# Kernel tuning notes

Measured on AMD Instinct MI355X. Metric: run time of the kernel, lower is better.

The kernel has to match this reference:

```python
import jax, jax.numpy as jnp
import numpy as np

B, S, D = 8, 4096, 256
N_INTENT, N_SLOT = 512, 1024


def setup_inputs() -> dict:
    key = jax.random.key(0)
    k1, k2, k3, k4 = jax.random.split(key, 4)
    return {
        "input_intent": jax.random.normal(k1, (B, S, D), dtype=jnp.float32),
        "input_slot": jax.random.normal(k2, (B, S, D), dtype=jnp.float32),
        "mask": jnp.ones((B, S), dtype=jnp.int32),  # unused, kept for API fidelity
        "W_intent_emb": jax.random.normal(k3, (N_INTENT, D), dtype=jnp.float32) * 0.02,
        "W_slot_emb": jax.random.normal(k4, (N_SLOT, D), dtype=jnp.float32) * 0.02,
    }


def reference(input_intent, input_slot, mask, W_intent_emb, W_slot_emb):
    # scores: [B, S, N] = hidden @ label_table^T
    intent_probs = jax.nn.softmax(jnp.einsum("bsd,nd->bsn", input_intent, W_intent_emb), axis=-1)
    slot_probs = jax.nn.softmax(jnp.einsum("bsd,nd->bsn", input_slot, W_slot_emb), axis=-1)
    # weighted sum over label embeddings: [B, S, D]
    intent_res = jnp.einsum("bsn,nd->bsd", intent_probs, W_intent_emb)
    slot_res = jnp.einsum("bsn,nd->bsd", slot_probs, W_slot_emb)
    return (intent_res, slot_res)
```

## Files before the change

### kernel.cpp

```cpp
#include <hip/hip_runtime.h>


#define TM 128
#define DD 256
#define THREADS 512
#define TOK 32768

typedef __bf16 bf16t;
typedef bf16t v8bf __attribute__((ext_vector_type(8)));
typedef float v16f __attribute__((ext_vector_type(16)));

#define WT0   0
#define WT1   32768
#define W20   65536
#define W21   98304
#define P_OFF 131072
#define L_OFF 147456
#define LDS_BYTES 147968

#define IWT 0
#define SWT 262144
#define IW2 786432
#define SW2 1048576

__device__ __forceinline__ unsigned short f2bf(float x) {
    unsigned u = __builtin_bit_cast(unsigned, x);
    unsigned r = u + 0x7fffu + ((u >> 16) & 1u);
    return (unsigned short)(r >> 16);
}

__global__ __launch_bounds__(256) void prep_w_kernel(
    const float* __restrict__ w_int, const float* __restrict__ w_slot,
    char* __restrict__ wsb)
{
    int t = blockIdx.x * 256 + threadIdx.x;
    int w = t >> 6, lane = t & 63;
    int hi = lane >> 5, l5 = lane & 31;
    union { unsigned short u[8]; uint4 q; } pk;

    if (w < 768) {
        int st   = (w >= 256);
        int widx = w - (st ? 256 : 0);
        int it = widx >> 5, fid = widx & 31;
        int wc = fid >> 4, kk = fid & 15;
        const float* W = st ? w_slot : w_int;
        int n  = it * 64 + wc * 32 + l5;
        int k0 = kk * 16 + hi * 8;
        #pragma unroll
        for (int j = 0; j < 8; ++j) pk.u[j] = f2bf(W[(size_t)n * DD + k0 + j]);
        char* dst = wsb + (st ? SWT : IWT) + (size_t)it * 32768 + fid * 1024 + lane * 16;
        *(uint4*)dst = pk.q;
    } else {
        int w2 = w - 768;
        int st   = (w2 >= 256);
        int widx = w2 - (st ? 256 : 0);
        int it = widx >> 5, fid = widx & 31;
        int kb = fid >> 3, db = fid & 7;
        const float* W = st ? w_slot : w_int;
        int n0 = it * 64 + kb * 16 + hi * 8;
        int d  = db * 32 + l5;
        #pragma unroll
        for (int j = 0; j < 8; ++j) pk.u[j] = f2bf(W[(size_t)(n0 + j) * DD + d]);
        char* dst = wsb + (st ? SW2 : IW2) + (size_t)it * 32768 + fid * 1024 + lane * 16;
        *(uint4*)dst = pk.q;
    }
}

__global__ __launch_bounds__(THREADS)
__attribute__((amdgpu_waves_per_eu(2, 2)))
void label_attn_kernel(
    const float* __restrict__ in_intent,
    const float* __restrict__ in_slot,
    const char* __restrict__ wsb,
    float* __restrict__ out)
{
    extern __shared__ char lds[];

    const int tid  = threadIdx.x;
    const int lane = tid & 63;
    const int wid  = tid >> 6;
    const int wr   = wid >> 1;
    const int wc   = wid & 1;
    const int hi   = lane >> 5;
    const int l5   = lane & 31;
    const int t0   = blockIdx.x * TM;

    float* lsf = (float*)(lds + L_OFF);

    const int kbl_w = (l5 >> 4) & 1;
    const int hb_w  = (l5 >> 3) & 1;
    const int pw_base = P_OFF + wr * 4096 + (wc * 2 + kbl_w) * 1024 + (l5 & 7) * 2;
    const int pw_sxor = (kbl_w << 2) ^ (hb_w << 1);

    for (int st = 0; st < 2; ++st) {
        __builtin_amdgcn_s_barrier();
        if (tid < TM) lsf[tid] = 0.0f;

        const float* __restrict__ inp = st ? in_slot : in_intent;
        const char*  __restrict__ wtg = wsb + (st ? SWT : IWT);
        const char*  __restrict__ w2g = wsb + (st ? SW2 : IW2);
        const int niter = st ? 16 : 8;
        float* __restrict__ outp = out + (size_t)st * TOK * DD;

        v8bf h[16];
        {
            const float* hp = inp + (size_t)(t0 + wr * 32 + l5) * DD + hi * 8;
            #pragma unroll
            for (int kk = 0; kk < 16; ++kk) {
                float4 a = *(const float4*)(hp + kk * 16);
                float4 b = *(const float4*)(hp + kk * 16 + 4);
                union { unsigned short u[8]; v8bf v; } pk;
                pk.u[0] = f2bf(a.x); pk.u[1] = f2bf(a.y);
                pk.u[2] = f2bf(a.z); pk.u[3] = f2bf(a.w);
                pk.u[4] = f2bf(b.x); pk.u[5] = f2bf(b.y);
                pk.u[6] = f2bf(b.z); pk.u[7] = f2bf(b.w);
                h[kk] = pk.v;
            }
        }

        #pragma unroll
        for (int c = 0; c < 4; ++c) {
            int chunk = wid * 4 + c;
            __builtin_amdgcn_global_load_lds(
                (const __attribute__((address_space(1))) unsigned*)(wtg + chunk * 1024 + lane * 16),
                (__attribute__((address_space(3))) unsigned*)(lds + WT0 + chunk * 1024),
                16, 0, 0);
        }
        __builtin_amdgcn_sched_barrier(0);
        #pragma unroll
        for (int c = 0; c < 4; ++c) {
            int chunk = wid * 4 + c;
            __builtin_amdgcn_global_load_lds(
                (const __attribute__((address_space(1))) unsigned*)(w2g + chunk * 1024 + lane * 16),
                (__attribute__((address_space(3))) unsigned*)(lds + W20 + chunk * 1024),
                16, 0, 0);
        }
        __builtin_amdgcn_sched_barrier(0);
        asm volatile("s_waitcnt vmcnt(0)" ::: "memory");
        __builtin_amdgcn_sched_barrier(0);
        __builtin_amdgcn_s_barrier();

        v16f  o[4] = {};
        float ls[16] = {};

        for (int it = 0; it < niter; ++it) {
            const int cur = it & 1;
            char* wt_buf = lds + (cur ? WT1 : WT0);
            char* w2_buf = lds + (cur ? W21 : W20);

            if (it + 1 < niter) {
                const char* s1 = wtg + (size_t)(it + 1) * 32768;
                const char* s2 = w2g + (size_t)(it + 1) * 32768;
                char* d1 = lds + (cur ? WT0 : WT1);
                char* d2 = lds + (cur ? W20 : W21);
                #pragma unroll
                for (int c = 0; c < 4; ++c) {
                    int chunk = wid * 4 + c;
                    __builtin_amdgcn_global_load_lds(
                        (const __attribute__((address_space(1))) unsigned*)(s1 + chunk * 1024 + lane * 16),
                        (__attribute__((address_space(3))) unsigned*)(d1 + chunk * 1024),
                        16, 0, 0);
                }
                __builtin_amdgcn_sched_barrier(0);
                #pragma unroll
                for (int c = 0; c < 4; ++c) {
                    int chunk = wid * 4 + c;
                    __builtin_amdgcn_global_load_lds(
                        (const __attribute__((address_space(1))) unsigned*)(s2 + chunk * 1024 + lane * 16),
                        (__attribute__((address_space(3))) unsigned*)(d2 + chunk * 1024),
                        16, 0, 0);
                }
                __builtin_amdgcn_sched_barrier(0);
            }

            v16f c0 = {}, c1 = {};
            #pragma unroll
            for (int kk = 0; kk < 16; kk += 2) {
                v8bf b0 = *(const v8bf*)(wt_buf + (wc * 16 + kk) * 1024 + lane * 16);
                v8bf b1 = *(const v8bf*)(wt_buf + (wc * 16 + kk + 1) * 1024 + lane * 16);
                c0 = __builtin_amdgcn_mfma_f32_32x32x16_bf16(h[kk],     b0, c0, 0, 0, 0);
                c1 = __builtin_amdgcn_mfma_f32_32x32x16_bf16(h[kk + 1], b1, c1, 0, 0, 0);
            }
            v16f cacc = c0 + c1;

            #pragma unroll
            for (int r = 0; r < 16; ++r) {
                int tl = (r & 3) + 8 * (r >> 2) + 4 * hi;
                float e = __expf(cacc[r]);
                unsigned short ub = f2bf(e);
                ls[r] += __builtin_bit_cast(float, ((unsigned)ub) << 16);
                int slot = (tl + 32 * hb_w) ^ pw_sxor;
                *(unsigned short*)(lds + pw_base + slot * 16) = ub;
            }

            if (it + 1 < niter) {
                asm volatile("s_waitcnt vmcnt(8)" ::: "memory");
            } else {
                asm volatile("s_waitcnt vmcnt(0)" ::: "memory");
            }
            asm volatile("s_waitcnt lgkmcnt(0)" ::: "memory");
            __builtin_amdgcn_sched_barrier(0);
            __builtin_amdgcn_s_barrier();

            #pragma unroll
            for (int kb = 0; kb < 4; ++kb) {
                int sl = lane ^ ((kb & 1) << 2) ^ (hi << 1);
                v8bf pa = *(const v8bf*)(lds + P_OFF + wr * 4096 + kb * 1024 + sl * 16);
                #pragma unroll
                for (int db = 0; db < 4; ++db) {
                    v8bf wb = *(const v8bf*)(w2_buf + (kb * 8 + wc * 4 + db) * 1024 + lane * 16);
                    o[db] = __builtin_amdgcn_mfma_f32_32x32x16_bf16(pa, wb, o[db], 0, 0, 0);
                }
            }

            if (it + 1 < niter) {
                asm volatile("s_waitcnt vmcnt(4)" ::: "memory");
            }
            __builtin_amdgcn_sched_barrier(0);
            __builtin_amdgcn_s_barrier();
        }

        #pragma unroll
        for (int r = 0; r < 16; ++r) {
            float s = ls[r];
            s += __shfl_xor(s, 1);
            s += __shfl_xor(s, 2);
            s += __shfl_xor(s, 4);
            s += __shfl_xor(s, 8);
            s += __shfl_xor(s, 16);
            ls[r] = s;
        }
        if (l5 == 0) {
            #pragma unroll
            for (int r = 0; r < 16; ++r) {
                int tl = (r & 3) + 8 * (r >> 2) + 4 * hi;
                atomicAdd(&lsf[wr * 32 + tl], ls[r]);
            }
        }
        __syncthreads();

        #pragma unroll
        for (int r = 0; r < 16; ++r) {
            int tl = (r & 3) + 8 * (r >> 2) + 4 * hi;
            float inv = 1.0f / lsf[wr * 32 + tl];
            size_t row = (size_t)(t0 + wr * 32 + tl);
            #pragma unroll
            for (int db = 0; db < 4; ++db)
                outp[row * DD + wc * 128 + db * 32 + l5] = o[db][r] * inv;
        }
    }
}

extern "C" void kernel_launch(void* const* d_in, const int* in_sizes, int n_in,
                              void* d_out, int out_size, void* d_ws, size_t ws_size,
                              hipStream_t stream) {
    const float* in_intent = (const float*)d_in[0];
    const float* in_slot   = (const float*)d_in[1];
    const float* w_intent  = (const float*)d_in[3];
    const float* w_slot    = (const float*)d_in[4];
    float* out = (float*)d_out;
    char* wsb = (char*)d_ws;

    (void)hipFuncSetAttribute((const void*)label_attn_kernel,
                              hipFuncAttributeMaxDynamicSharedMemorySize, LDS_BYTES);

    prep_w_kernel<<<384, 256, 0, stream>>>(w_intent, w_slot, wsb);

    label_attn_kernel<<<dim3(TOK / TM, 1, 1), dim3(THREADS, 1, 1), LDS_BYTES, stream>>>(
        in_intent, in_slot, wsb, out);
}
```

Baseline: 179.3 us.

## Keep softmax probabilities in registers via lane shuffles, split N across wave pairs

Computes the score tile transposed (weights as A operand) so each lane's exp'd probabilities can be packed and exchanged with a cross-half shuffle to form the second MFMA's A operand directly. This removes the P round trip through LDS and one barrier per iteration. Each wave pair now splits the label dimension rather than the output D dimension, so each wave accumulates all 256 output columns (twice the accumulator registers) and the halves are reduced through LDS at the end. The weight prefetch is issued before the input conversion, and the per-iteration wait becomes a full vmcnt(0), which may expose prefetch latency and raise register pressure.

```diff
diff --git a/kernel.cpp b/kernel.cpp
--- a/kernel.cpp
+++ b/kernel.cpp
@@ -14,9 +14,8 @@
 #define WT1   32768
 #define W20   65536
 #define W21   98304
-#define P_OFF 131072
-#define L_OFF 147456
-#define LDS_BYTES 147968
+#define L_OFF 131072
+#define LDS_BYTES 131584
 
 #define IWT 0
 #define SWT 262144
@@ -87,11 +86,6 @@
 
     float* lsf = (float*)(lds + L_OFF);
 
-    const int kbl_w = (l5 >> 4) & 1;
-    const int hb_w  = (l5 >> 3) & 1;
-    const int pw_base = P_OFF + wr * 4096 + (wc * 2 + kbl_w) * 1024 + (l5 & 7) * 2;
-    const int pw_sxor = (kbl_w << 2) ^ (hb_w << 1);
-
     for (int st = 0; st < 2; ++st) {
         __builtin_amdgcn_s_barrier();
         if (tid < TM) lsf[tid] = 0.0f;
@@ -101,6 +95,25 @@
         const char*  __restrict__ w2g = wsb + (st ? SW2 : IW2);
         const int niter = st ? 16 : 8;
         float* __restrict__ outp = out + (size_t)st * TOK * DD;
+
+        #pragma unroll
+        for (int c = 0; c < 4; ++c) {
+            int chunk = wid * 4 + c;
+            __builtin_amdgcn_global_load_lds(
+                (const __attribute__((address_space(1))) unsigned*)(wtg + chunk * 1024 + lane * 16),
+                (__attribute__((address_space(3))) unsigned*)(lds + WT0 + chunk * 1024),
+                16, 0, 0);
+        }
+        __builtin_amdgcn_sched_barrier(0);
+        #pragma unroll
+        for (int c = 0; c < 4; ++c) {
+            int chunk = wid * 4 + c;
+            __builtin_amdgcn_global_load_lds(
+                (const __attribute__((address_space(1))) unsigned*)(w2g + chunk * 1024 + lane * 16),
+                (__attribute__((address_space(3))) unsigned*)(lds + W20 + chunk * 1024),
+                16, 0, 0);
+        }
+        __builtin_amdgcn_sched_barrier(0);
 
         v8bf h[16];
         {
@@ -118,41 +131,22 @@
             }
         }
 
-        #pragma unroll
-        for (int c = 0; c < 4; ++c) {
-            int chunk = wid * 4 + c;
-            __builtin_amdgcn_global_load_lds(
-                (const __attribute__((address_space(1))) unsigned*)(wtg + chunk * 1024 + lane * 16),
-                (__attribute__((address_space(3))) unsigned*)(lds + WT0 + chunk * 1024),
-                16, 0, 0);
-        }
-        __builtin_amdgcn_sched_barrier(0);
-        #pragma unroll
-        for (int c = 0; c < 4; ++c) {
-            int chunk = wid * 4 + c;
-            __builtin_amdgcn_global_load_lds(
-                (const __attribute__((address_space(1))) unsigned*)(w2g + chunk * 1024 + lane * 16),
-                (__attribute__((address_space(3))) unsigned*)(lds + W20 + chunk * 1024),
-                16, 0, 0);
-        }
-        __builtin_amdgcn_sched_barrier(0);
         asm volatile("s_waitcnt vmcnt(0)" ::: "memory");
         __builtin_amdgcn_sched_barrier(0);
         __builtin_amdgcn_s_barrier();
 
-        v16f  o[4] = {};
-        float ls[16] = {};
+        v16f  o[8] = {};
+        float ls = 0.0f;
 
         for (int it = 0; it < niter; ++it) {
-            const int cur = it & 1;
-            char* wt_buf = lds + (cur ? WT1 : WT0);
-            char* w2_buf = lds + (cur ? W21 : W20);
+            char* wt_buf = lds + ((it & 1) ? WT1 : WT0);
+            char* w2_buf = lds + ((it & 1) ? W21 : W20);
 
             if (it + 1 < niter) {
                 const char* s1 = wtg + (size_t)(it + 1) * 32768;
                 const char* s2 = w2g + (size_t)(it + 1) * 32768;
-                char* d1 = lds + (cur ? WT0 : WT1);
-                char* d2 = lds + (cur ? W20 : W21);
+                char* d1 = lds + ((it & 1) ? WT0 : WT1);
+                char* d2 = lds + ((it & 1) ? W20 : W21);
                 #pragma unroll
                 for (int c = 0; c < 4; ++c) {
                     int chunk = wid * 4 + c;
@@ -161,7 +155,6 @@
                         (__attribute__((address_space(3))) unsigned*)(d1 + chunk * 1024),
                         16, 0, 0);
                 }
-                __builtin_amdgcn_sched_barrier(0);
                 #pragma unroll
                 for (int c = 0; c < 4; ++c) {
                     int chunk = wid * 4 + c;
@@ -173,80 +166,78 @@
                 __builtin_amdgcn_sched_barrier(0);
             }
 
-            v16f c0 = {}, c1 = {};
-            #pragma unroll
-            for (int kk = 0; kk < 16; kk += 2) {
-                v8bf b0 = *(const v8bf*)(wt_buf + (wc * 16 + kk) * 1024 + lane * 16);
-                v8bf b1 = *(const v8bf*)(wt_buf + (wc * 16 + kk + 1) * 1024 + lane * 16);
-                c0 = __builtin_amdgcn_mfma_f32_32x32x16_bf16(h[kk],     b0, c0, 0, 0, 0);
-                c1 = __builtin_amdgcn_mfma_f32_32x32x16_bf16(h[kk + 1], b1, c1, 0, 0, 0);
-            }
-            v16f cacc = c0 + c1;
-
+            v16f cacc = {};
+            #pragma unroll
+            for (int kk = 0; kk < 16; ++kk) {
+                v8bf a = *(const v8bf*)(wt_buf + (wc * 16 + kk) * 1024 + lane * 16);
+                cacc = __builtin_amdgcn_mfma_f32_32x32x16_bf16(a, h[kk], cacc, 0, 0, 0);
+            }
+
+            unsigned pkq[8];
+            #pragma unroll
+            for (int q = 0; q < 4; ++q) {
+                unsigned short u0 = f2bf(__expf(cacc[4 * q + 0]));
+                unsigned short u1 = f2bf(__expf(cacc[4 * q + 1]));
+                unsigned short u2 = f2bf(__expf(cacc[4 * q + 2]));
+                unsigned short u3 = f2bf(__expf(cacc[4 * q + 3]));
+                ls += __builtin_bit_cast(float, ((unsigned)u0) << 16);
+                ls += __builtin_bit_cast(float, ((unsigned)u1) << 16);
+                ls += __builtin_bit_cast(float, ((unsigned)u2) << 16);
+                ls += __builtin_bit_cast(float, ((unsigned)u3) << 16);
+                pkq[2 * q]     = (unsigned)u0 | ((unsigned)u1 << 16);
+                pkq[2 * q + 1] = (unsigned)u2 | ((unsigned)u3 << 16);
+            }
+            unsigned oth[8];
+            #pragma unroll
+            for (int i = 0; i < 8; ++i)
+                oth[i] = (unsigned)__shfl_xor((int)pkq[i], 32);
+
+            #pragma unroll
+            for (int kb = 0; kb < 2; ++kb) {
+                uint4 sel;
+                sel.x = hi ? oth[4 * kb + 2] : pkq[4 * kb + 0];
+                sel.y = hi ? oth[4 * kb + 3] : pkq[4 * kb + 1];
+                sel.z = hi ? pkq[4 * kb + 2] : oth[4 * kb + 0];
+                sel.w = hi ? pkq[4 * kb + 3] : oth[4 * kb + 1];
+                v8bf pa = __builtin_bit_cast(v8bf, sel);
+                #pragma unroll
+                for (int db = 0; db < 8; ++db) {
+                    v8bf wb = *(const v8bf*)(w2_buf + ((wc * 2 + kb) * 8 + db) * 1024 + lane * 16);
+                    o[db] = __builtin_amdgcn_mfma_f32_32x32x16_bf16(pa, wb, o[db], 0, 0, 0);
+                }
+            }
+
+            asm volatile("s_waitcnt vmcnt(0)" ::: "memory");
+            __builtin_amdgcn_sched_barrier(0);
+            __builtin_amdgcn_s_barrier();
+        }
+
+        float s = ls + __shfl_xor(ls, 32);
+        if (lane < 32) atomicAdd(&lsf[wr * 32 + lane], s);
+
+        if (wc == 0) {
+            float* reg = (float*)(lds + wr * 32768);
+            #pragma unroll
+            for (int db = 0; db < 8; ++db)
+                #pragma unroll
+                for (int r = 0; r < 16; ++r)
+                    reg[(db * 16 + r) * 64 + lane] = o[db][r];
+        }
+        __syncthreads();
+
+        if (wc == 1) {
+            const float* reg = (const float*)(lds + wr * 32768);
             #pragma unroll
             for (int r = 0; r < 16; ++r) {
                 int tl = (r & 3) + 8 * (r >> 2) + 4 * hi;
-                float e = __expf(cacc[r]);
-                unsigned short ub = f2bf(e);
-                ls[r] += __builtin_bit_cast(float, ((unsigned)ub) << 16);
-                int slot = (tl + 32 * hb_w) ^ pw_sxor;
-                *(unsigned short*)(lds + pw_base + slot * 16) = ub;
-            }
-
-            if (it + 1 < niter) {
-                asm volatile("s_waitcnt vmcnt(8)" ::: "memory");
-            } else {
-                asm volatile("s_waitcnt vmcnt(0)" ::: "memory");
-            }
-            asm volatile("s_waitcnt lgkmcnt(0)" ::: "memory");
-            __builtin_amdgcn_sched_barrier(0);
-            __builtin_amdgcn_s_barrier();
-
-            #pragma unroll
-            for (int kb = 0; kb < 4; ++kb) {
-                int sl = lane ^ ((kb & 1) << 2) ^ (hi << 1);
-                v8bf pa = *(const v8bf*)(lds + P_OFF + wr * 4096 + kb * 1024 + sl * 16);
-                #pragma unroll
-                for (int db = 0; db < 4; ++db) {
-                    v8bf wb = *(const v8bf*)(w2_buf + (kb * 8 + wc * 4 + db) * 1024 + lane * 16);
-                    o[db] = __builtin_amdgcn_mfma_f32_32x32x16_bf16(pa, wb, o[db], 0, 0, 0);
-                }
-            }
-
-            if (it + 1 < niter) {
-                asm volatile("s_waitcnt vmcnt(4)" ::: "memory");
-            }
-            __builtin_amdgcn_sched_barrier(0);
-            __builtin_amdgcn_s_barrier();
-        }
-
-        #pragma unroll
-        for (int r = 0; r < 16; ++r) {
-            float s = ls[r];
-            s += __shfl_xor(s, 1);
-            s += __shfl_xor(s, 2);
-            s += __shfl_xor(s, 4);
-            s += __shfl_xor(s, 8);
-            s += __shfl_xor(s, 16);
-            ls[r] = s;
-        }
-        if (l5 == 0) {
-            #pragma unroll
-            for (int r = 0; r < 16; ++r) {
-                int tl = (r & 3) + 8 * (r >> 2) + 4 * hi;
-                atomicAdd(&lsf[wr * 32 + tl], ls[r]);
-            }
-        }
-        __syncthreads();
-
-        #pragma unroll
-        for (int r = 0; r < 16; ++r) {
-            int tl = (r & 3) + 8 * (r >> 2) + 4 * hi;
-            float inv = 1.0f / lsf[wr * 32 + tl];
-            size_t row = (size_t)(t0 + wr * 32 + tl);
-            #pragma unroll
-            for (int db = 0; db < 4; ++db)
-                outp[row * DD + wc * 128 + db * 32 + l5] = o[db][r] * inv;
+                float inv = 1.0f / lsf[wr * 32 + tl];
+                size_t row = (size_t)(t0 + wr * 32 + tl);
+                #pragma unroll
+                for (int db = 0; db < 8; ++db) {
+                    float tot = o[db][r] + reg[(db * 16 + r) * 64 + lane];
+                    outp[row * DD + db * 32 + l5] = tot * inv;
+                }
+            }
         }
     }
 }
```

Result: slower. 191.6 us (+6.9%).
